# Performance work log

Measured on AMD Instinct MI355X. Metric: run time of the kernel, lower is better.

The kernel has to match this reference:

```python
import jax, jax.numpy as jnp
import numpy as np

B, ENC_IN, ENC_HID, N, GH = 64, 64, 256, 2048, 128
LN_EPS = 1e-5


def _chain_adjacency(n):
    # tridiagonal chain adjacency, D^{-1/2} A D^{-1/2} normalized
    off = jnp.ones((n - 1,), dtype=jnp.float32)
    A = jnp.diag(off, 1) + jnp.diag(off, -1)
    deg = A.sum(axis=1)
    d_inv_sqrt = jnp.power(deg + 1e-8, -0.5)
    return A * d_inv_sqrt[None, :] * d_inv_sqrt[:, None]


def setup_inputs() -> dict:
    key = jax.random.key(0)
    ks = jax.random.split(key, 16)
    s = 0.02
    return {
        "x": jax.random.normal(ks[0], (B, ENC_IN), dtype=jnp.float32),
        "A_hat": _chain_adjacency(N),
        "W1": jax.random.normal(ks[1], (ENC_IN, ENC_HID), dtype=jnp.float32) * s,
        "b1": jnp.zeros((ENC_HID,), dtype=jnp.float32),
        "W2": jax.random.normal(ks[2], (ENC_HID, N * GH), dtype=jnp.float32) * s,
        "b2": jnp.zeros((N * GH,), dtype=jnp.float32),
        "Wg1": jax.random.normal(ks[3], (GH, GH), dtype=jnp.float32) * s,
        "Wg2": jax.random.normal(ks[4], (GH, GH), dtype=jnp.float32) * s,
        "ln_g1": jnp.ones((GH,), dtype=jnp.float32),
        "ln_b1": jnp.zeros((GH,), dtype=jnp.float32),
        "ln_g2": jnp.ones((GH,), dtype=jnp.float32),
        "ln_b2": jnp.zeros((GH,), dtype=jnp.float32),
        "Wout": jax.random.normal(ks[5], (GH, 1), dtype=jnp.float32) * s,
        "bout": jnp.zeros((1,), dtype=jnp.float32),
    }


def _layernorm(h, g, b):
    mu = h.mean(axis=-1, keepdims=True)
    var = ((h - mu) ** 2).mean(axis=-1, keepdims=True)
    return (h - mu) * jax.lax.rsqrt(var + LN_EPS) * g + b


def reference(x, A_hat, W1, b1, W2, b2, Wg1, Wg2, ln_g1, ln_b1, ln_g2, ln_b2, Wout, bout):
    # encoder MLP -> (B, N, GH) node features
    enc = jax.nn.relu(x @ W1 + b1) @ W2 + b2
    out = enc.reshape(B, N, GH)
    # GCN layers: out = out + A_hat @ (LN(out) W)   (dropout is identity at eval)
    for Wg, g, bb in ((Wg1, ln_g1, ln_b1), (Wg2, ln_g2, ln_b2)):
        h = _layernorm(out, g, bb)
        Wx = h @ Wg                              # (B, N, GH)
        out = out + jnp.einsum('ij,bjd->bid', A_hat, Wx)
    return (out @ Wout + bout).squeeze(-1)       # (B, N)
```

## Files before the change

### kernel.cpp

```cpp
#include <hip/hip_runtime.h>


#define B_    64
#define EIN   64
#define EHID  256
#define NN    2048
#define GH    128
#define NG    (NN*GH)
#define LN_EPS 1e-5f
#define C3    28
#define C4    128

typedef _Float16 f16;
typedef _Float16 f16x8 __attribute__((ext_vector_type(8)));
typedef _Float16 f16x4 __attribute__((ext_vector_type(4)));
typedef float    f32x4 __attribute__((ext_vector_type(4)));
typedef unsigned int u32;

#define AS1 __attribute__((address_space(1)))
#define AS3 __attribute__((address_space(3)))

__device__ __forceinline__ float wred(float v) {
#pragma unroll
    for (int off = 32; off > 0; off >>= 1) v += __shfl_xor(v, off, 64);
    return v;
}

__global__ __launch_bounds__(256) void k_prep(
    const float* __restrict__ x,  const float* __restrict__ W1, const float* __restrict__ b1,
    const float* __restrict__ Wg1,const float* __restrict__ Wg2,const float* __restrict__ Wout,
    f16* __restrict__ h1h, f16* __restrict__ wg1T, float* __restrict__ v2)
{
    int bid = blockIdx.x, tid = threadIdx.x;
    if (bid < 64) {
        int b = bid, j = tid;
        float acc = b1[j];
#pragma unroll 8
        for (int k = 0; k < EIN; ++k) acc = fmaf(x[b*EIN + k], W1[k*EHID + j], acc);
        h1h[b*EHID + j] = (f16)fmaxf(acc, 0.f);
    } else if (bid == 64) {
        if (tid < GH) {
            float s = 0.f;
            for (int j = 0; j < GH; ++j) s = fmaf(Wg2[tid*GH + j], Wout[j], s);
            v2[tid] = s;
        }
    } else {
        for (int i = tid; i < GH*GH; i += 256) {
            int n = i >> 7, k = i & 127;
            wg1T[i] = (f16)Wg1[k*GH + n];
        }
    }
}

__global__ __launch_bounds__(256) void k_enc(
    const float* __restrict__ W2, const float* __restrict__ b2,
    const f16* __restrict__ h1h, f16* __restrict__ out0)
{
    __shared__ float w2s[2][32][128];

    int tid = threadIdx.x;
    int L = tid & 63, wv = tid >> 6, hi = L >> 4, lo = L & 15;
    int c0 = blockIdx.x * 128;
    int lrow = L >> 5, lcol4 = (L & 31) * 4;

    auto stage = [&](int kk, int nb) {
#pragma unroll
        for (int s = 0; s < 4; ++s) {
            int r = wv*8 + s*2;
            const float* gp = W2 + (size_t)(kk*32 + r + lrow) * NG + c0 + lcol4;
            __builtin_amdgcn_global_load_lds((const AS1 void*)gp,
                                             (AS3 void*)&w2s[nb][r][0], 16, 0, 0);
        }
    };

    stage(0, 0);

    f32x4 acc[4][2];
#pragma unroll
    for (int bg = 0; bg < 4; ++bg)
#pragma unroll
        for (int t = 0; t < 2; ++t) acc[bg][t] = f32x4{0.f, 0.f, 0.f, 0.f};

#pragma unroll
    for (int kk = 0; kk < 8; ++kk) {
        __syncthreads();
        if (kk < 7) stage(kk + 1, (kk + 1) & 1);

        const float (*wb)[128] = w2s[kk & 1];
        f16x8 bf[2];
#pragma unroll
        for (int t = 0; t < 2; ++t)
#pragma unroll
            for (int j = 0; j < 8; ++j)
                bf[t][j] = (f16)wb[hi*8 + j][wv*32 + t*16 + lo];

        f16x8 af[4];
#pragma unroll
        for (int bg = 0; bg < 4; ++bg)
            af[bg] = *(const f16x8*)(h1h + ((bg*16 + lo) << 8) + kk*32 + hi*8);

#pragma unroll
        for (int bg = 0; bg < 4; ++bg)
#pragma unroll
            for (int t = 0; t < 2; ++t)
                acc[bg][t] = __builtin_amdgcn_mfma_f32_16x16x32_f16(af[bg], bf[t], acc[bg][t], 0, 0, 0);
    }

    float bv[2];
#pragma unroll
    for (int t = 0; t < 2; ++t) bv[t] = b2[c0 + wv*32 + t*16 + lo];
#pragma unroll
    for (int bg = 0; bg < 4; ++bg)
#pragma unroll
        for (int t = 0; t < 2; ++t)
#pragma unroll
            for (int r = 0; r < 4; ++r) {
                int brow = bg*16 + hi*4 + r;
                out0[(size_t)brow * NG + c0 + wv*32 + t*16 + lo] = (f16)(acc[bg][t][r] + bv[t]);
            }
}

__global__ __launch_bounds__(256) void k_gcn1(
    const float* __restrict__ A_hat, const float* __restrict__ ln_g1, const float* __restrict__ ln_b1,
    const f16* __restrict__ wg1T, const f16* __restrict__ out0, f16* __restrict__ out1)
{
    __shared__ f16 out0_s[32][132];
    __shared__ f16 h0s[32][136];
    __shared__ f16 wx0_s[32][132];
    __shared__ float g1s[GH], b1s[GH];
    __shared__ float clo_s[C3], chi_s[C3];

    int tid = threadIdx.x;
    int n0 = blockIdx.x * C3;
    int b  = blockIdx.y;

    for (int i = tid; i < 32*32; i += 256) {
        int r = i >> 5, gv = i & 31;
        int n = n0 - 2 + r;
        f16x4 v = {0, 0, 0, 0};
        if (n >= 0 && n < NN) v = *(const f16x4*)(out0 + ((size_t)b*NN + n)*GH + gv*4);
        *(f16x4*)&out0_s[r][gv*4] = v;
    }
    if (tid < GH) { g1s[tid] = ln_g1[tid]; b1s[tid] = ln_b1[tid]; }
    else if (tid < GH + C3) {
        int t = tid - GH, n = n0 + t;
        float cl = 0.f, ch = 0.f;
        if (n < NN) {
            if (n >= 1)    cl = A_hat[(size_t)n*NN + (n-1)];
            if (n <= NN-2) ch = A_hat[(size_t)n*NN + (n+1)];
        }
        clo_s[t] = cl; chi_s[t] = ch;
    }
    __syncthreads();

    int L = tid & 63, wv = tid >> 6, hi = L >> 4, lo = L & 15;
    for (int r = wv; r < 32; r += 4) {
        float x0 = (float)out0_s[r][2*L], x1 = (float)out0_s[r][2*L+1];
        float s  = wred(x0 + x1);
        float q  = wred(x0*x0 + x1*x1);
        float mu = s * (1.f/128.f);
        float inv = rsqrtf(q*(1.f/128.f) - mu*mu + LN_EPS);
        h0s[r][2*L]   = (f16)((x0 - mu)*inv*g1s[2*L]   + b1s[2*L]);
        h0s[r][2*L+1] = (f16)((x1 - mu)*inv*g1s[2*L+1] + b1s[2*L+1]);
    }
    __syncthreads();

    f32x4 z = {0.f, 0.f, 0.f, 0.f};
    f32x4 acc[2][2];
#pragma unroll
    for (int mg = 0; mg < 2; ++mg)
#pragma unroll
        for (int nt = 0; nt < 2; ++nt) acc[mg][nt] = z;

#pragma unroll
    for (int kk = 0; kk < 4; ++kk) {
        f16x8 af[2], bfr[2];
#pragma unroll
        for (int mg = 0; mg < 2; ++mg)
            af[mg] = *(const f16x8*)&h0s[mg*16 + lo][kk*32 + hi*8];
#pragma unroll
        for (int nt = 0; nt < 2; ++nt) {
            int n = wv*32 + nt*16 + lo;
            bfr[nt] = *(const f16x8*)(wg1T + n*GH + kk*32 + hi*8);
        }
#pragma unroll
        for (int mg = 0; mg < 2; ++mg)
#pragma unroll
            for (int nt = 0; nt < 2; ++nt)
                acc[mg][nt] = __builtin_amdgcn_mfma_f32_16x16x32_f16(af[mg], bfr[nt], acc[mg][nt], 0, 0, 0);
    }
#pragma unroll
    for (int mg = 0; mg < 2; ++mg)
#pragma unroll
        for (int nt = 0; nt < 2; ++nt)
#pragma unroll
            for (int r = 0; r < 4; ++r)
                wx0_s[mg*16 + hi*4 + r][wv*32 + nt*16 + lo] = (f16)acc[mg][nt][r];
    __syncthreads();

    for (int i = tid; i < C3*GH; i += 256) {
        int t = i >> 7, g = i & 127;
        int n = n0 + t;
        if (n < NN) {
            float val = (float)out0_s[t+2][g]
                      + clo_s[t]*(float)wx0_s[t+1][g]
                      + chi_s[t]*(float)wx0_s[t+3][g];
            out1[((size_t)b*NN + n)*GH + g] = (f16)val;
        }
    }
}

__global__ __launch_bounds__(256) void k_gcn2(
    const float* __restrict__ A_hat, const float* __restrict__ ln_g2, const float* __restrict__ ln_b2,
    const float* __restrict__ Wout, const float* __restrict__ bout, const float* __restrict__ v2,
    const f16* __restrict__ out1, float* __restrict__ y)
{
    __shared__ f16 out1_s[C4+2][132];
    __shared__ float g2s[GH], b2s[GH], v2s[GH], wos[GH];
    __shared__ float ss[C4+2], yr[C4+2];

    int tid = threadIdx.x;
    int n0 = blockIdx.x * C4;
    int b  = blockIdx.y;

    for (int i = tid; i < (C4+2)*32; i += 256) {
        int r = i >> 5, gv = i & 31;
        int n = n0 - 1 + r;
        f16x4 v = {0, 0, 0, 0};
        if (n >= 0 && n < NN) v = *(const f16x4*)(out1 + ((size_t)b*NN + n)*GH + gv*4);
        *(f16x4*)&out1_s[r][gv*4] = v;
    }
    if (tid < GH) { g2s[tid] = ln_g2[tid]; b2s[tid] = ln_b2[tid]; v2s[tid] = v2[tid]; wos[tid] = Wout[tid]; }
    __syncthreads();

    int L = tid & 63, wv = tid >> 6;
    for (int r = wv; r < C4+2; r += 4) {
        float x0 = (float)out1_s[r][2*L], x1 = (float)out1_s[r][2*L+1];
        float s  = wred(x0 + x1);
        float q  = wred(x0*x0 + x1*x1);
        float mu = s * (1.f/128.f);
        float inv = rsqrtf(q*(1.f/128.f) - mu*mu + LN_EPS);
        float h0 = (x0 - mu)*inv*g2s[2*L]   + b2s[2*L];
        float h1 = (x1 - mu)*inv*g2s[2*L+1] + b2s[2*L+1];
        float sp = wred(h0*v2s[2*L] + h1*v2s[2*L+1]);
        float yp = wred(x0*wos[2*L] + x1*wos[2*L+1]);
        if (L == 0) { ss[r] = sp; yr[r] = yp; }
    }
    __syncthreads();

    if (tid < C4) {
        int n = n0 + tid, r = tid + 1;
        float cl = (n >= 1)    ? A_hat[(size_t)n*NN + (n-1)] : 0.f;
        float ch = (n <= NN-2) ? A_hat[(size_t)n*NN + (n+1)] : 0.f;
        y[(size_t)b*NN + n] = yr[r] + bout[0] + cl*ss[r-1] + ch*ss[r+1];
    }
}

extern "C" void kernel_launch(void* const* d_in, const int* in_sizes, int n_in,
                              void* d_out, int out_size, void* d_ws, size_t ws_size,
                              hipStream_t stream)
{
    (void)in_sizes; (void)n_in; (void)out_size; (void)ws_size;
    const float* x    = (const float*)d_in[0];
    const float* A_hat= (const float*)d_in[1];
    const float* W1   = (const float*)d_in[2];
    const float* b1   = (const float*)d_in[3];
    const float* W2   = (const float*)d_in[4];
    const float* b2   = (const float*)d_in[5];
    const float* Wg1  = (const float*)d_in[6];
    const float* Wg2  = (const float*)d_in[7];
    const float* g1   = (const float*)d_in[8];
    const float* lb1  = (const float*)d_in[9];
    const float* g2   = (const float*)d_in[10];
    const float* lb2  = (const float*)d_in[11];
    const float* Wout = (const float*)d_in[12];
    const float* bout = (const float*)d_in[13];
    float* y = (float*)d_out;

    char* ws = (char*)d_ws;
    f16*   h1h  = (f16*)(ws + 0);
    f16*   wg1T = (f16*)(ws + 32768);
    float* v2   = (float*)(ws + 65536);
    f16*   out0 = (f16*)(ws + (1u << 20));
    f16*   out1 = (f16*)(ws + (1u << 20) + (size_t)B_*NG*2);

    k_prep<<<dim3(66),                    256, 0, stream>>>(x, W1, b1, Wg1, Wg2, Wout, h1h, wg1T, v2);
    k_enc <<<dim3(NG/128),                256, 0, stream>>>(W2, b2, h1h, out0);
    k_gcn1<<<dim3((NN + C3 - 1)/C3, B_),  256, 0, stream>>>(A_hat, g1, lb1, wg1T, out0, out1);
    k_gcn2<<<dim3(NN/C4, B_),             256, 0, stream>>>(A_hat, g2, lb2, Wout, bout, v2, out1, y);
}
```

Measured before the change: 500.1 us.

## Fuse both GCN layers into one kernel and pad encoder LDS tile

Merges the two GCN kernels into one. Each block now computes the layer-1 result for its 30 halo rows in shared memory and applies the layer-2 LayerNorm and projection directly, so the f16 out1 intermediate is never written to or read back from global memory. The chain-adjacency coefficients are extracted once in the prep kernel into small arrays instead of being gathered from A_hat in every block. The encoder's LDS staging buffer for W2 is also padded (516-float row groups) to reduce bank conflicts on the transposed reads.

```diff
diff --git a/kernel.cpp b/kernel.cpp
--- a/kernel.cpp
+++ b/kernel.cpp
@@ -9,7 +9,6 @@
 #define NG    (NN*GH)
 #define LN_EPS 1e-5f
 #define C3    28
-#define C4    128
 
 typedef _Float16 f16;
 typedef _Float16 f16x8 __attribute__((ext_vector_type(8)));
@@ -29,7 +28,9 @@
 __global__ __launch_bounds__(256) void k_prep(
     const float* __restrict__ x,  const float* __restrict__ W1, const float* __restrict__ b1,
     const float* __restrict__ Wg1,const float* __restrict__ Wg2,const float* __restrict__ Wout,
-    f16* __restrict__ h1h, f16* __restrict__ wg1T, float* __restrict__ v2)
+    const float* __restrict__ A_hat,
+    f16* __restrict__ h1h, f16* __restrict__ wg1T, float* __restrict__ v2,
+    float* __restrict__ clo, float* __restrict__ chi)
 {
     int bid = blockIdx.x, tid = threadIdx.x;
     if (bid < 64) {
@@ -44,11 +45,15 @@
             for (int j = 0; j < GH; ++j) s = fmaf(Wg2[tid*GH + j], Wout[j], s);
             v2[tid] = s;
         }
-    } else {
+    } else if (bid == 65) {
         for (int i = tid; i < GH*GH; i += 256) {
             int n = i >> 7, k = i & 127;
             wg1T[i] = (f16)Wg1[k*GH + n];
         }
+    } else {
+        int n = (bid - 66) * 256 + tid;
+        clo[n] = (n >= 1)    ? A_hat[(size_t)n*NN + (n-1)] : 0.f;
+        chi[n] = (n <= NN-2) ? A_hat[(size_t)n*NN + (n+1)] : 0.f;
     }
 }
 
@@ -56,7 +61,7 @@
     const float* __restrict__ W2, const float* __restrict__ b2,
     const f16* __restrict__ h1h, f16* __restrict__ out0)
 {
-    __shared__ float w2s[2][32][128];
+    __shared__ float w2s[2][4128];
 
     int tid = threadIdx.x;
     int L = tid & 63, wv = tid >> 6, hi = L >> 4, lo = L & 15;
@@ -68,8 +73,8 @@
         for (int s = 0; s < 4; ++s) {
             int r = wv*8 + s*2;
             const float* gp = W2 + (size_t)(kk*32 + r + lrow) * NG + c0 + lcol4;
-            __builtin_amdgcn_global_load_lds((const AS1 void*)gp,
-                                             (AS3 void*)&w2s[nb][r][0], 16, 0, 0);
+            float* ldst = &w2s[nb][(r >> 2)*516 + (r & 3)*128];
+            __builtin_amdgcn_global_load_lds((const AS1 void*)gp, (AS3 void*)ldst, 16, 0, 0);
         }
     };
 
@@ -86,13 +91,13 @@
         __syncthreads();
         if (kk < 7) stage(kk + 1, (kk + 1) & 1);
 
-        const float (*wb)[128] = w2s[kk & 1];
+        const float* wb = w2s[kk & 1];
         f16x8 bf[2];
 #pragma unroll
         for (int t = 0; t < 2; ++t)
 #pragma unroll
             for (int j = 0; j < 8; ++j)
-                bf[t][j] = (f16)wb[hi*8 + j][wv*32 + t*16 + lo];
+                bf[t][j] = (f16)wb[(hi*2 + (j >> 2))*516 + (j & 3)*128 + wv*32 + t*16 + lo];
 
         f16x8 af[4];
 #pragma unroll
@@ -120,15 +125,20 @@
             }
 }
 
-__global__ __launch_bounds__(256) void k_gcn1(
-    const float* __restrict__ A_hat, const float* __restrict__ ln_g1, const float* __restrict__ ln_b1,
-    const f16* __restrict__ wg1T, const f16* __restrict__ out0, f16* __restrict__ out1)
+__global__ __launch_bounds__(256) void k_gcn(
+    const float* __restrict__ clo, const float* __restrict__ chi,
+    const float* __restrict__ ln_g1, const float* __restrict__ ln_b1,
+    const float* __restrict__ ln_g2, const float* __restrict__ ln_b2,
+    const float* __restrict__ Wout, const float* __restrict__ bout,
+    const float* __restrict__ v2, const f16* __restrict__ wg1T,
+    const f16* __restrict__ out0, float* __restrict__ y)
 {
     __shared__ f16 out0_s[32][132];
     __shared__ f16 h0s[32][136];
     __shared__ f16 wx0_s[32][132];
-    __shared__ float g1s[GH], b1s[GH];
-    __shared__ float clo_s[C3], chi_s[C3];
+    __shared__ float g1s[GH], b1s[GH], g2s[GH], b2s[GH], v2s[GH], wos[GH];
+    __shared__ float cls[32], chs[32];
+    __shared__ float ss[32], yrs[32];
 
     int tid = threadIdx.x;
     int n0 = blockIdx.x * C3;
@@ -141,15 +151,15 @@
         if (n >= 0 && n < NN) v = *(const f16x4*)(out0 + ((size_t)b*NN + n)*GH + gv*4);
         *(f16x4*)&out0_s[r][gv*4] = v;
     }
-    if (tid < GH) { g1s[tid] = ln_g1[tid]; b1s[tid] = ln_b1[tid]; }
-    else if (tid < GH + C3) {
-        int t = tid - GH, n = n0 + t;
-        float cl = 0.f, ch = 0.f;
-        if (n < NN) {
-            if (n >= 1)    cl = A_hat[(size_t)n*NN + (n-1)];
-            if (n <= NN-2) ch = A_hat[(size_t)n*NN + (n+1)];
-        }
-        clo_s[t] = cl; chi_s[t] = ch;
+    if (tid < GH) {
+        g1s[tid] = ln_g1[tid]; b1s[tid] = ln_b1[tid];
+        g2s[tid] = ln_g2[tid]; b2s[tid] = ln_b2[tid];
+        v2s[tid] = v2[tid];    wos[tid] = Wout[tid];
+    } else if (tid < GH + 32) {
+        int r = tid - GH, n = n0 - 2 + r;
+        bool ok = (n >= 0 && n < NN);
+        cls[r] = ok ? clo[n] : 0.f;
+        chs[r] = ok ? chi[n] : 0.f;
     }
     __syncthreads();
 
@@ -165,12 +175,11 @@
     }
     __syncthreads();
 
-    f32x4 z = {0.f, 0.f, 0.f, 0.f};
     f32x4 acc[2][2];
 #pragma unroll
     for (int mg = 0; mg < 2; ++mg)
 #pragma unroll
-        for (int nt = 0; nt < 2; ++nt) acc[mg][nt] = z;
+        for (int nt = 0; nt < 2; ++nt) acc[mg][nt] = f32x4{0.f, 0.f, 0.f, 0.f};
 
 #pragma unroll
     for (int kk = 0; kk < 4; ++kk) {
@@ -198,44 +207,17 @@
                 wx0_s[mg*16 + hi*4 + r][wv*32 + nt*16 + lo] = (f16)acc[mg][nt][r];
     __syncthreads();
 
-    for (int i = tid; i < C3*GH; i += 256) {
-        int t = i >> 7, g = i & 127;
-        int n = n0 + t;
-        if (n < NN) {
-            float val = (float)out0_s[t+2][g]
-                      + clo_s[t]*(float)wx0_s[t+1][g]
-                      + chi_s[t]*(float)wx0_s[t+3][g];
-            out1[((size_t)b*NN + n)*GH + g] = (f16)val;
-        }
-    }
-}
-
-__global__ __launch_bounds__(256) void k_gcn2(
-    const float* __restrict__ A_hat, const float* __restrict__ ln_g2, const float* __restrict__ ln_b2,
-    const float* __restrict__ Wout, const float* __restrict__ bout, const float* __restrict__ v2,
-    const f16* __restrict__ out1, float* __restrict__ y)
-{
-    __shared__ f16 out1_s[C4+2][132];
-    __shared__ float g2s[GH], b2s[GH], v2s[GH], wos[GH];
-    __shared__ float ss[C4+2], yr[C4+2];
-
-    int tid = threadIdx.x;
-    int n0 = blockIdx.x * C4;
-    int b  = blockIdx.y;
-
-    for (int i = tid; i < (C4+2)*32; i += 256) {
-        int r = i >> 5, gv = i & 31;
-        int n = n0 - 1 + r;
-        f16x4 v = {0, 0, 0, 0};
-        if (n >= 0 && n < NN) v = *(const f16x4*)(out1 + ((size_t)b*NN + n)*GH + gv*4);
-        *(f16x4*)&out1_s[r][gv*4] = v;
-    }
-    if (tid < GH) { g2s[tid] = ln_g2[tid]; b2s[tid] = ln_b2[tid]; v2s[tid] = v2[tid]; wos[tid] = Wout[tid]; }
-    __syncthreads();
-
-    int L = tid & 63, wv = tid >> 6;
-    for (int r = wv; r < C4+2; r += 4) {
-        float x0 = (float)out1_s[r][2*L], x1 = (float)out1_s[r][2*L+1];
+    for (int i = tid; i < 30*GH; i += 256) {
+        int r = 1 + (i >> 7), g = i & 127;
+        float val = (float)out0_s[r][g]
+                  + cls[r]*(float)wx0_s[r-1][g]
+                  + chs[r]*(float)wx0_s[r+1][g];
+        out0_s[r][g] = (f16)val;
+    }
+    __syncthreads();
+
+    for (int r = 1 + wv; r <= 30; r += 4) {
+        float x0 = (float)out0_s[r][2*L], x1 = (float)out0_s[r][2*L+1];
         float s  = wred(x0 + x1);
         float q  = wred(x0*x0 + x1*x1);
         float mu = s * (1.f/128.f);
@@ -244,15 +226,16 @@
         float h1 = (x1 - mu)*inv*g2s[2*L+1] + b2s[2*L+1];
         float sp = wred(h0*v2s[2*L] + h1*v2s[2*L+1]);
         float yp = wred(x0*wos[2*L] + x1*wos[2*L+1]);
-        if (L == 0) { ss[r] = sp; yr[r] = yp; }
-    }
-    __syncthreads();
-
-    if (tid < C4) {
-        int n = n0 + tid, r = tid + 1;
-        float cl = (n >= 1)    ? A_hat[(size_t)n*NN + (n-1)] : 0.f;
-        float ch = (n <= NN-2) ? A_hat[(size_t)n*NN + (n+1)] : 0.f;
-        y[(size_t)b*NN + n] = yr[r] + bout[0] + cl*ss[r-1] + ch*ss[r+1];
+        if (L == 0) { ss[r] = sp; yrs[r] = yp; }
+    }
+    __syncthreads();
+
+    if (tid < C3) {
+        int n = n0 + tid;
+        if (n < NN) {
+            int r = tid + 2;
+            y[(size_t)b*NN + n] = yrs[r] + bout[0] + cls[r]*ss[r-1] + chs[r]*ss[r+1];
+        }
     }
 }
 
@@ -281,11 +264,13 @@
     f16*   h1h  = (f16*)(ws + 0);
     f16*   wg1T = (f16*)(ws + 32768);
     float* v2   = (float*)(ws + 65536);
+    float* clo  = (float*)(ws + 81920);
+    float* chi  = (float*)(ws + 90112);
     f16*   out0 = (f16*)(ws + (1u << 20));
-    f16*   out1 = (f16*)(ws + (1u << 20) + (size_t)B_*NG*2);
-
-    k_prep<<<dim3(66),                    256, 0, stream>>>(x, W1, b1, Wg1, Wg2, Wout, h1h, wg1T, v2);
-    k_enc <<<dim3(NG/128),                256, 0, stream>>>(W2, b2, h1h, out0);
-    k_gcn1<<<dim3((NN + C3 - 1)/C3, B_),  256, 0, stream>>>(A_hat, g1, lb1, wg1T, out0, out1);
-    k_gcn2<<<dim3(NN/C4, B_),             256, 0, stream>>>(A_hat, g2, lb2, Wout, bout, v2, out1, y);
-}
+
+    k_prep<<<dim3(74),                   256, 0, stream>>>(x, W1, b1, Wg1, Wg2, Wout, A_hat,
+                                                           h1h, wg1T, v2, clo, chi);
+    k_enc <<<dim3(NG/128),               256, 0, stream>>>(W2, b2, h1h, out0);
+    k_gcn <<<dim3((NN + C3 - 1)/C3, B_), 256, 0, stream>>>(clo, chi, g1, lb1, g2, lb2,
+                                                           Wout, bout, v2, wg1T, out0, y);
+}
```

New measurement: 486.2 us. 1.03x faster.
